# Performance work log

Measured on AMD Instinct MI355X. Metric: run time of the kernel, lower is better.

## Reference

```python
import jax, jax.numpy as jnp
import numpy as np

D_MODEL = 1024
NUM_HEADS = 16
HEAD_DIM = D_MODEL // NUM_HEADS


def setup_inputs() -> dict:
    key = jax.random.key(0)
    ks = jax.random.split(key, 9)
    B, S = 4, 2048
    scale = 1.0 / np.sqrt(D_MODEL)
    x = jax.random.normal(ks[0], (B, S, D_MODEL), dtype=jnp.float32)
    Wq = jax.random.normal(ks[1], (D_MODEL, D_MODEL), dtype=jnp.float32) * scale
    bq = jnp.zeros((D_MODEL,), dtype=jnp.float32)
    Wk = jax.random.normal(ks[2], (D_MODEL, D_MODEL), dtype=jnp.float32) * scale
    bk = jnp.zeros((D_MODEL,), dtype=jnp.float32)
    Wv = jax.random.normal(ks[3], (D_MODEL, D_MODEL), dtype=jnp.float32) * scale
    bv = jnp.zeros((D_MODEL,), dtype=jnp.float32)
    Wo = jax.random.normal(ks[4], (D_MODEL, D_MODEL), dtype=jnp.float32) * scale
    bo = jnp.zeros((D_MODEL,), dtype=jnp.float32)
    mask = jnp.ones((B, S), dtype=jnp.int32)  # 1 = attend, 0 = masked out
    return {"x": x, "mask": mask, "Wq": Wq, "bq": bq, "Wk": Wk, "bk": bk,
            "Wv": Wv, "bv": bv, "Wo": Wo, "bo": bo}


def reference(x, mask, Wq, bq, Wk, bk, Wv, bv, Wo, bo):
    B, S, D = x.shape
    H, Hd = NUM_HEADS, HEAD_DIM
    # torch Linear: y = x @ W.T + b
    q = (jnp.einsum('bsd,ed->bse', x, Wq) + bq).reshape(B, S, H, Hd).transpose(0, 2, 1, 3)
    k = (jnp.einsum('bsd,ed->bse', x, Wk) + bk).reshape(B, S, H, Hd).transpose(0, 2, 1, 3)
    v = (jnp.einsum('bsd,ed->bse', x, Wv) + bv).reshape(B, S, H, Hd).transpose(0, 2, 1, 3)
    # scaled dot-product attention with key padding mask [B,1,1,S]
    scores = jnp.einsum('bhqd,bhkd->bhqk', q, k) / jnp.sqrt(jnp.float32(Hd))
    m = mask[:, None, None, :]
    scores = jnp.where(m == 0, jnp.float32(-jnp.inf), scores)
    attn = jax.nn.softmax(scores, axis=-1)
    vals = jnp.einsum('bhqk,bhkd->bhqd', attn, v)
    vals = vals.transpose(0, 2, 1, 3).reshape(B, S, D)
    out = jnp.einsum('bsd,ed->bse', vals, Wo) + bo
    return out
```

## Files before the change

### kernel.cpp

```cpp
#include <hip/hip_runtime.h>
#include <hip/hip_bf16.h>

typedef __attribute__((ext_vector_type(8))) short short8;
typedef __attribute__((ext_vector_type(4))) short short4b;
typedef __attribute__((ext_vector_type(4))) int int4v;
typedef __attribute__((ext_vector_type(4))) float f32x4;

#define MFMA_BF16(A_, B_, C_) __builtin_amdgcn_mfma_f32_16x16x32_bf16((A_), (B_), (C_), 0, 0, 0)

#if defined(__HIP_DEVICE_COMPILE__)
#if __has_builtin(__builtin_amdgcn_exp2f)
__device__ __forceinline__ float exp2_nat(float x) { return __builtin_amdgcn_exp2f(x); }
#else
__device__ __forceinline__ float exp2_nat(float x) {
  float r;
  asm("v_exp_f32 %0, %1" : "=v"(r) : "v"(x));
  return r;
}
#endif
#else
__device__ __forceinline__ float exp2_nat(float x) { return exp2f(x); }
#endif

__device__ __forceinline__ unsigned short f2bf(float f) {
  unsigned int u = __builtin_bit_cast(unsigned int, f);
  return (unsigned short)((u + 0x7FFFu + ((u >> 16) & 1u)) >> 16);
}

__device__ __forceinline__ void gll16(const unsigned short* g, unsigned short* l) {
  __builtin_amdgcn_global_load_lds((const __attribute__((address_space(1))) void*)g,
                                   (__attribute__((address_space(3))) void*)l, 16, 0, 0);
}

#define NX (8192 * 1024)
#define NW (1024 * 1024)

__global__ void convert_k(const float* __restrict__ x,
                          const float* __restrict__ wq, const float* __restrict__ wk,
                          const float* __restrict__ wv, const float* __restrict__ wo,
                          unsigned short* __restrict__ xb,
                          unsigned short* __restrict__ wqkv,
                          unsigned short* __restrict__ wob) {
  size_t i = ((size_t)blockIdx.x * blockDim.x + threadIdx.x) * 4;
  const float* sp;
  unsigned short* dp;
  if (i < (size_t)NX) {
    sp = x + i; dp = xb + i;
  } else {
    size_t j = i - NX;
    if (j < (size_t)NW)               { sp = wq + j;            dp = wqkv + j; }
    else if (j < (size_t)(2 * NW))    { sp = wk + (j - NW);     dp = wqkv + j; }
    else if (j < (size_t)(3 * NW))    { sp = wv + (j - 2 * NW); dp = wqkv + j; }
    else                              { sp = wo + (j - 3 * NW); dp = wob + (j - 3 * NW); }
  }
  float4 v = *(const float4*)sp;
  ushort4 o;
  o.x = f2bf(v.x); o.y = f2bf(v.y); o.z = f2bf(v.z); o.w = f2bf(v.w);
  *(ushort4*)dp = o;
}

__global__ __launch_bounds__(256, 2) void gemm_qkv_k(
    const unsigned short* __restrict__ A, const unsigned short* __restrict__ Bw,
    const float* __restrict__ bq, const float* __restrict__ bk, const float* __restrict__ bv,
    unsigned short* __restrict__ qb, unsigned short* __restrict__ kb,
    unsigned short* __restrict__ vtb) {
  const int K = 1024;
  __shared__ __align__(16) unsigned short lA[128 * 32];
  __shared__ __align__(16) unsigned short lB[128 * 32];
  const int tid = threadIdx.x;
  const int lane = tid & 63;
  const int w = tid >> 6;
  const int wm = w >> 1, wn = w & 1;
  const int m0 = blockIdx.x * 128, n0 = blockIdx.y * 128;
  const int l15 = lane & 15, lg = lane >> 4;

  const f32x4 zf = {0.0f, 0.0f, 0.0f, 0.0f};
  f32x4 acc[4][4];
#pragma unroll
  for (int mi = 0; mi < 4; ++mi)
#pragma unroll
    for (int ni = 0; ni < 4; ++ni) acc[mi][ni] = zf;

  const int c0 = tid, c1 = tid + 256;
  const int r0 = c0 >> 2, k0c = (c0 & 3) * 8;
  const int r1 = c1 >> 2, k1c = (c1 & 3) * 8;
  const unsigned short* ga0 = A + (size_t)(m0 + r0) * K + k0c;
  const unsigned short* ga1 = A + (size_t)(m0 + r1) * K + k1c;
  const unsigned short* gb0 = Bw + (size_t)(n0 + r0) * K + k0c;
  const unsigned short* gb1 = Bw + (size_t)(n0 + r1) * K + k1c;

  for (int kt = 0; kt < K; kt += 32) {
    __syncthreads();
    gll16(ga0 + kt, lA + c0 * 8);
    gll16(ga1 + kt, lA + c1 * 8);
    gll16(gb0 + kt, lB + c0 * 8);
    gll16(gb1 + kt, lB + c1 * 8);
    __syncthreads();
    short8 af[4], bf[4];
#pragma unroll
    for (int mi = 0; mi < 4; ++mi)
      af[mi] = *(const short8*)&lA[(wm * 64 + mi * 16 + l15) * 32 + lg * 8];
#pragma unroll
    for (int ni = 0; ni < 4; ++ni)
      bf[ni] = *(const short8*)&lB[(wn * 64 + ni * 16 + l15) * 32 + lg * 8];
#pragma unroll
    for (int mi = 0; mi < 4; ++mi)
#pragma unroll
      for (int ni = 0; ni < 4; ++ni)
        acc[mi][ni] = MFMA_BF16(af[mi], bf[ni], acc[mi][ni]);
  }

  const int which = n0 >> 10;
  const float* bias = (which == 0) ? bq : (which == 1) ? bk : bv;
  const float qs = (which == 0) ? 0.125f * 1.44269504088896f : 1.0f;
#pragma unroll
  for (int ni = 0; ni < 4; ++ni) {
    const int n = n0 + wn * 64 + ni * 16 + l15;
    const int nn = n & 1023;
    const float bia = bias[nn];
    const int h = nn >> 6, hd = nn & 63;
#pragma unroll
    for (int mi = 0; mi < 4; ++mi) {
      const int mb = m0 + wm * 64 + mi * 16 + lg * 4;
      const int b = mb >> 11, s = mb & 2047;
      const int bh = b * 16 + h;
      if (which < 2) {
        unsigned short* dst = ((which == 0) ? qb : kb) + ((size_t)bh * 2048 + s) * 64 + hd;
#pragma unroll
        for (int r = 0; r < 4; ++r)
          dst[(size_t)r * 64] = f2bf((acc[mi][ni][r] + bia) * qs);
      } else {
        const int tle = s >> 6, w64 = s & 63;
        const int f = w64 >> 4, lgk = (w64 >> 2) & 3;
        const int kvp0 = (f >> 1) * 32 + lgk * 8 + (f & 1) * 4;
        ushort4 pk;
        pk.x = f2bf(acc[mi][ni][0] + bia);
        pk.y = f2bf(acc[mi][ni][1] + bia);
        pk.z = f2bf(acc[mi][ni][2] + bia);
        pk.w = f2bf(acc[mi][ni][3] + bia);
        *(ushort4*)(vtb + (((size_t)bh * 32 + tle) * 64 + hd) * 64 + kvp0) = pk;
      }
    }
  }
}

__global__ __launch_bounds__(256, 4) void attn_k(
    const unsigned short* __restrict__ Qb, const unsigned short* __restrict__ Kb,
    const unsigned short* __restrict__ VTb, const int* __restrict__ mask,
    unsigned short* __restrict__ vals) {
  __shared__ __align__(16) unsigned short Kl[2][64 * 64];
  __shared__ __align__(16) unsigned short Vl[2][64 * 64];
  const int tid = threadIdx.x;
  const int lane = tid & 63;
  const int w = tid >> 6;
  const int l15 = lane & 15, lg = lane >> 4;

  const int bid = blockIdx.x;
  const int wk = (bid & 7) * 128 + (bid >> 3);
  const int bh = wk >> 4, qt = wk & 15;
  const int b = bh >> 4, h = bh & 15;
  const int q0 = qt * 128 + w * 32;

  const unsigned short* Qp = Qb + (size_t)bh * (2048 * 64);
  const int* mp = mask + b * 2048;

  int mOk = 1;
  {
    const int4v* mq = (const int4v*)mp;
#pragma unroll
    for (int i = 0; i < 8; ++i) {
      int4v m = mq[lane * 8 + i];
      mOk &= (m[0] != 0) & (m[1] != 0) & (m[2] != 0) & (m[3] != 0);
    }
  }
  const bool maskAll = __all(mOk != 0);

  const int srow = tid >> 3;
  const int scol = ((tid & 7) ^ (srow & 7)) * 8;
  const unsigned short* kSrc = Kb + (size_t)bh * (2048 * 64) + srow * 64 + scol;
  const unsigned short* vSrc = VTb + (size_t)bh * (32 * 64 * 64) + srow * 64 + scol;

  short8 qf[2][2];
#pragma unroll
  for (int mi = 0; mi < 2; ++mi)
#pragma unroll
    for (int ks = 0; ks < 2; ++ks)
      qf[mi][ks] = *(const short8*)(Qp + (size_t)(q0 + mi * 16 + l15) * 64 + ks * 32 + lg * 8);

  const f32x4 zf = {0.0f, 0.0f, 0.0f, 0.0f};
  const short8 ones8 = {(short)0x3F80, (short)0x3F80, (short)0x3F80, (short)0x3F80,
                        (short)0x3F80, (short)0x3F80, (short)0x3F80, (short)0x3F80};
  f32x4 acc[2][4];
  f32x4 lsum[2];
#pragma unroll
  for (int mi = 0; mi < 2; ++mi) {
#pragma unroll
    for (int hf = 0; hf < 4; ++hf) acc[mi][hf] = zf;
    lsum[mi] = zf;
  }

  gll16(kSrc, &Kl[0][tid * 8]);
  gll16(kSrc + 2048, &Kl[0][tid * 8 + 2048]);
  gll16(vSrc, &Vl[0][tid * 8]);
  gll16(vSrc + 2048, &Vl[0][tid * 8 + 2048]);
  __syncthreads();

  for (int t = 0; t < 32; ++t) {
    const int cur = t & 1;
    if (t < 31) {
      const size_t off = (size_t)(t + 1) * 4096;
      unsigned short* kd = &Kl[cur ^ 1][tid * 8];
      unsigned short* vd = &Vl[cur ^ 1][tid * 8];
      gll16(kSrc + off, kd);
      gll16(kSrc + off + 2048, kd + 2048);
      gll16(vSrc + off, vd);
      gll16(vSrc + off + 2048, vd + 2048);
    }
    const unsigned short* Kc = Kl[cur];
    const unsigned short* Vc = Vl[cur];
    const int kv0 = t * 64;

    int4v mv[4];
    if (!maskAll) {
#pragma unroll
      for (int f = 0; f < 4; ++f) mv[f] = *(const int4v*)(mp + kv0 + f * 16 + lg * 4);
    }

    f32x4 sc[2][4];
    __builtin_amdgcn_s_setprio(1);
#pragma unroll
    for (int f = 0; f < 4; ++f) {
      short8 kf0 = *(const short8*)&Kc[(f * 16 + l15) * 64 + ((lg ^ (l15 & 7)) * 8)];
      short8 kf1 = *(const short8*)&Kc[(f * 16 + l15) * 64 + (((4 + lg) ^ (l15 & 7)) * 8)];
#pragma unroll
      for (int mi = 0; mi < 2; ++mi) {
        f32x4 tq = MFMA_BF16(kf0, qf[mi][0], zf);
        sc[mi][f] = MFMA_BF16(kf1, qf[mi][1], tq);
      }
    }
    __builtin_amdgcn_s_setprio(0);

    short8 pb[2][2];
#pragma unroll
    for (int mi = 0; mi < 2; ++mi)
#pragma unroll
      for (int f = 0; f < 4; ++f)
#pragma unroll
        for (int r = 0; r < 4; ++r) {
          float p = exp2_nat(sc[mi][f][r]);
          if (!maskAll) p = (mv[f][r] != 0) ? p : 0.0f;
          __hip_bfloat16 hb = __float2bfloat16(p);
          pb[mi][f >> 1][(f & 1) * 4 + r] = (short)__builtin_bit_cast(unsigned short, hb);
        }

    __builtin_amdgcn_s_setprio(1);
#pragma unroll
    for (int mi = 0; mi < 2; ++mi)
#pragma unroll
      for (int pr = 0; pr < 2; ++pr)
        lsum[mi] = MFMA_BF16(ones8, pb[mi][pr], lsum[mi]);
#pragma unroll
    for (int hf = 0; hf < 4; ++hf) {
#pragma unroll
      for (int pr = 0; pr < 2; ++pr) {
        short8 vv = *(const short8*)&Vc[(hf * 16 + l15) * 64 + (((pr * 4 + lg) ^ (l15 & 7)) * 8)];
#pragma unroll
        for (int mi = 0; mi < 2; ++mi)
          acc[mi][hf] = MFMA_BF16(vv, pb[mi][pr], acc[mi][hf]);
      }
    }
    __builtin_amdgcn_s_setprio(0);

    __syncthreads();
  }

#pragma unroll
  for (int mi = 0; mi < 2; ++mi) {
    float inv = 1.0f / lsum[mi][0];
    const int q = q0 + mi * 16 + l15;
    unsigned short* dst = vals + ((size_t)b * 2048 + q) * 1024 + h * 64 + lg * 4;
#pragma unroll
    for (int hf = 0; hf < 4; ++hf) {
      ushort4 o;
      o.x = f2bf(acc[mi][hf][0] * inv);
      o.y = f2bf(acc[mi][hf][1] * inv);
      o.z = f2bf(acc[mi][hf][2] * inv);
      o.w = f2bf(acc[mi][hf][3] * inv);
      *(ushort4*)(dst + hf * 16) = o;
    }
  }
}

__global__ __launch_bounds__(256, 2) void gemm_out_k(
    const unsigned short* __restrict__ A, const unsigned short* __restrict__ Bw,
    const float* __restrict__ bo, float* __restrict__ out) {
  const int K = 1024;
  __shared__ __align__(16) unsigned short lA[128 * 32];
  __shared__ __align__(16) unsigned short lB[128 * 32];
  const int tid = threadIdx.x;
  const int lane = tid & 63;
  const int w = tid >> 6;
  const int wm = w >> 1, wn = w & 1;
  const int m0 = blockIdx.x * 128, n0 = blockIdx.y * 128;
  const int l15 = lane & 15, lg = lane >> 4;

  const f32x4 zf = {0.0f, 0.0f, 0.0f, 0.0f};
  f32x4 acc[4][4];
#pragma unroll
  for (int mi = 0; mi < 4; ++mi)
#pragma unroll
    for (int ni = 0; ni < 4; ++ni) acc[mi][ni] = zf;

  const int c0 = tid, c1 = tid + 256;
  const int r0 = c0 >> 2, k0c = (c0 & 3) * 8;
  const int r1 = c1 >> 2, k1c = (c1 & 3) * 8;
  const unsigned short* ga0 = A + (size_t)(m0 + r0) * K + k0c;
  const unsigned short* ga1 = A + (size_t)(m0 + r1) * K + k1c;
  const unsigned short* gb0 = Bw + (size_t)(n0 + r0) * K + k0c;
  const unsigned short* gb1 = Bw + (size_t)(n0 + r1) * K + k1c;

  for (int kt = 0; kt < K; kt += 32) {
    __syncthreads();
    gll16(ga0 + kt, lA + c0 * 8);
    gll16(ga1 + kt, lA + c1 * 8);
    gll16(gb0 + kt, lB + c0 * 8);
    gll16(gb1 + kt, lB + c1 * 8);
    __syncthreads();
    short8 af[4], bf[4];
#pragma unroll
    for (int mi = 0; mi < 4; ++mi)
      af[mi] = *(const short8*)&lA[(wm * 64 + mi * 16 + l15) * 32 + lg * 8];
#pragma unroll
    for (int ni = 0; ni < 4; ++ni)
      bf[ni] = *(const short8*)&lB[(wn * 64 + ni * 16 + l15) * 32 + lg * 8];
#pragma unroll
    for (int mi = 0; mi < 4; ++mi)
#pragma unroll
      for (int ni = 0; ni < 4; ++ni)
        acc[mi][ni] = MFMA_BF16(af[mi], bf[ni], acc[mi][ni]);
  }

#pragma unroll
  for (int ni = 0; ni < 4; ++ni) {
    const int n = n0 + wn * 64 + ni * 16 + l15;
    const float bia = bo[n];
#pragma unroll
    for (int mi = 0; mi < 4; ++mi) {
      const int mb = m0 + wm * 64 + mi * 16 + lg * 4;
#pragma unroll
      for (int r = 0; r < 4; ++r)
        out[(size_t)(mb + r) * 1024 + n] = acc[mi][ni][r] + bia;
    }
  }
}

extern "C" void kernel_launch(void* const* d_in, const int* in_sizes, int n_in,
                              void* d_out, int out_size, void* d_ws, size_t ws_size,
                              hipStream_t stream) {
  const float* x  = (const float*)d_in[0];
  const int* mask = (const int*)d_in[1];
  const float* Wq = (const float*)d_in[2];
  const float* bq = (const float*)d_in[3];
  const float* Wk = (const float*)d_in[4];
  const float* bk = (const float*)d_in[5];
  const float* Wv = (const float*)d_in[6];
  const float* bv = (const float*)d_in[7];
  const float* Wo = (const float*)d_in[8];
  const float* bo = (const float*)d_in[9];
  float* out = (float*)d_out;

  unsigned short* xb   = (unsigned short*)d_ws;
  unsigned short* wqkv = xb + (size_t)8192 * 1024;
  unsigned short* wob  = wqkv + (size_t)3072 * 1024;
  unsigned short* qb   = wob + (size_t)1024 * 1024;
  unsigned short* kb   = qb + (size_t)64 * 2048 * 64;
  unsigned short* vtb  = kb + (size_t)64 * 2048 * 64;
  unsigned short* vals = vtb + (size_t)64 * 2048 * 64;

  convert_k<<<dim3(12288), dim3(256), 0, stream>>>(x, Wq, Wk, Wv, Wo, xb, wqkv, wob);
  gemm_qkv_k<<<dim3(64, 24), dim3(256), 0, stream>>>(xb, wqkv, bq, bk, bv, qb, kb, vtb);
  attn_k<<<dim3(1024), dim3(256), 0, stream>>>(qb, kb, vtb, mask, vals);
  gemm_out_k<<<dim3(64, 8), dim3(256), 0, stream>>>(vals, wob, bo, out);
}
```

Before: 193.8 us.

## Double GEMM K-tile to 64 with XOR-swizzled LDS layout; unroll attention loop

Both projection GEMMs now stage a 64-wide K slice per iteration instead of 32, which halves the number of barrier pairs per output tile. Global-to-LDS copies write into an XOR-swizzled column layout so the 16-lane fragment reads avoid LDS bank conflicts. The attention KV loop also gets an unroll-by-2 pragma. LDS per block doubles to 32 KB, which may limit occupancy, and the copy and compute phases are still not overlapped.

```diff
diff --git a/kernel.cpp b/kernel.cpp
--- a/kernel.cpp
+++ b/kernel.cpp
@@ -65,8 +65,8 @@
     unsigned short* __restrict__ qb, unsigned short* __restrict__ kb,
     unsigned short* __restrict__ vtb) {
   const int K = 1024;
-  __shared__ __align__(16) unsigned short lA[128 * 32];
-  __shared__ __align__(16) unsigned short lB[128 * 32];
+  __shared__ __align__(16) unsigned short lA[128 * 64];
+  __shared__ __align__(16) unsigned short lB[128 * 64];
   const int tid = threadIdx.x;
   const int lane = tid & 63;
   const int w = tid >> 6;
@@ -81,33 +81,39 @@
 #pragma unroll
     for (int ni = 0; ni < 4; ++ni) acc[mi][ni] = zf;
 
-  const int c0 = tid, c1 = tid + 256;
-  const int r0 = c0 >> 2, k0c = (c0 & 3) * 8;
-  const int r1 = c1 >> 2, k1c = (c1 & 3) * 8;
-  const unsigned short* ga0 = A + (size_t)(m0 + r0) * K + k0c;
-  const unsigned short* ga1 = A + (size_t)(m0 + r1) * K + k1c;
-  const unsigned short* gb0 = Bw + (size_t)(n0 + r0) * K + k0c;
-  const unsigned short* gb1 = Bw + (size_t)(n0 + r1) * K + k1c;
-
-  for (int kt = 0; kt < K; kt += 32) {
-    __syncthreads();
-    gll16(ga0 + kt, lA + c0 * 8);
-    gll16(ga1 + kt, lA + c1 * 8);
-    gll16(gb0 + kt, lB + c0 * 8);
-    gll16(gb1 + kt, lB + c1 * 8);
-    __syncthreads();
-    short8 af[4], bf[4];
-#pragma unroll
-    for (int mi = 0; mi < 4; ++mi)
-      af[mi] = *(const short8*)&lA[(wm * 64 + mi * 16 + l15) * 32 + lg * 8];
-#pragma unroll
-    for (int ni = 0; ni < 4; ++ni)
-      bf[ni] = *(const short8*)&lB[(wn * 64 + ni * 16 + l15) * 32 + lg * 8];
-#pragma unroll
-    for (int mi = 0; mi < 4; ++mi)
+  const int srow = tid >> 3;
+  const int scol = ((tid & 7) ^ (srow & 7)) * 8;
+  const unsigned short* gA[4];
+  const unsigned short* gB[4];
+#pragma unroll
+  for (int q = 0; q < 4; ++q) {
+    gA[q] = A + (size_t)(m0 + q * 32 + srow) * K + scol;
+    gB[q] = Bw + (size_t)(n0 + q * 32 + srow) * K + scol;
+  }
+
+  for (int kt = 0; kt < K; kt += 64) {
+    __syncthreads();
+#pragma unroll
+    for (int q = 0; q < 4; ++q) {
+      gll16(gA[q] + kt, lA + q * 2048 + tid * 8);
+      gll16(gB[q] + kt, lB + q * 2048 + tid * 8);
+    }
+    __syncthreads();
+#pragma unroll
+    for (int ks = 0; ks < 2; ++ks) {
+      short8 af[4], bf[4];
+#pragma unroll
+      for (int mi = 0; mi < 4; ++mi)
+        af[mi] = *(const short8*)&lA[(wm * 64 + mi * 16 + l15) * 64 + (((ks * 4 + lg) ^ (l15 & 7)) * 8)];
 #pragma unroll
       for (int ni = 0; ni < 4; ++ni)
-        acc[mi][ni] = MFMA_BF16(af[mi], bf[ni], acc[mi][ni]);
+        bf[ni] = *(const short8*)&lB[(wn * 64 + ni * 16 + l15) * 64 + (((ks * 4 + lg) ^ (l15 & 7)) * 8)];
+#pragma unroll
+      for (int mi = 0; mi < 4; ++mi)
+#pragma unroll
+        for (int ni = 0; ni < 4; ++ni)
+          acc[mi][ni] = MFMA_BF16(af[mi], bf[ni], acc[mi][ni]);
+    }
   }
 
   const int which = n0 >> 10;
@@ -205,6 +211,7 @@
   gll16(vSrc + 2048, &Vl[0][tid * 8 + 2048]);
   __syncthreads();
 
+#pragma unroll 2
   for (int t = 0; t < 32; ++t) {
     const int cur = t & 1;
     if (t < 31) {
@@ -295,8 +302,8 @@
     const unsigned short* __restrict__ A, const unsigned short* __restrict__ Bw,
     const float* __restrict__ bo, float* __restrict__ out) {
   const int K = 1024;
-  __shared__ __align__(16) unsigned short lA[128 * 32];
-  __shared__ __align__(16) unsigned short lB[128 * 32];
+  __shared__ __align__(16) unsigned short lA[128 * 64];
+  __shared__ __align__(16) unsigned short lB[128 * 64];
   const int tid = threadIdx.x;
   const int lane = tid & 63;
   const int w = tid >> 6;
@@ -311,33 +318,39 @@
 #pragma unroll
     for (int ni = 0; ni < 4; ++ni) acc[mi][ni] = zf;
 
-  const int c0 = tid, c1 = tid + 256;
-  const int r0 = c0 >> 2, k0c = (c0 & 3) * 8;
-  const int r1 = c1 >> 2, k1c = (c1 & 3) * 8;
-  const unsigned short* ga0 = A + (size_t)(m0 + r0) * K + k0c;
-  const unsigned short* ga1 = A + (size_t)(m0 + r1) * K + k1c;
-  const unsigned short* gb0 = Bw + (size_t)(n0 + r0) * K + k0c;
-  const unsigned short* gb1 = Bw + (size_t)(n0 + r1) * K + k1c;
-
-  for (int kt = 0; kt < K; kt += 32) {
-    __syncthreads();
-    gll16(ga0 + kt, lA + c0 * 8);
-    gll16(ga1 + kt, lA + c1 * 8);
-    gll16(gb0 + kt, lB + c0 * 8);
-    gll16(gb1 + kt, lB + c1 * 8);
-    __syncthreads();
-    short8 af[4], bf[4];
-#pragma unroll
-    for (int mi = 0; mi < 4; ++mi)
-      af[mi] = *(const short8*)&lA[(wm * 64 + mi * 16 + l15) * 32 + lg * 8];
-#pragma unroll
-    for (int ni = 0; ni < 4; ++ni)
-      bf[ni] = *(const short8*)&lB[(wn * 64 + ni * 16 + l15) * 32 + lg * 8];
-#pragma unroll
-    for (int mi = 0; mi < 4; ++mi)
+  const int srow = tid >> 3;
+  const int scol = ((tid & 7) ^ (srow & 7)) * 8;
+  const unsigned short* gA[4];
+  const unsigned short* gB[4];
+#pragma unroll
+  for (int q = 0; q < 4; ++q) {
+    gA[q] = A + (size_t)(m0 + q * 32 + srow) * K + scol;
+    gB[q] = Bw + (size_t)(n0 + q * 32 + srow) * K + scol;
+  }
+
+  for (int kt = 0; kt < K; kt += 64) {
+    __syncthreads();
+#pragma unroll
+    for (int q = 0; q < 4; ++q) {
+      gll16(gA[q] + kt, lA + q * 2048 + tid * 8);
+      gll16(gB[q] + kt, lB + q * 2048 + tid * 8);
+    }
+    __syncthreads();
+#pragma unroll
+    for (int ks = 0; ks < 2; ++ks) {
+      short8 af[4], bf[4];
+#pragma unroll
+      for (int mi = 0; mi < 4; ++mi)
+        af[mi] = *(const short8*)&lA[(wm * 64 + mi * 16 + l15) * 64 + (((ks * 4 + lg) ^ (l15 & 7)) * 8)];
 #pragma unroll
       for (int ni = 0; ni < 4; ++ni)
-        acc[mi][ni] = MFMA_BF16(af[mi], bf[ni], acc[mi][ni]);
+        bf[ni] = *(const short8*)&lB[(wn * 64 + ni * 16 + l15) * 64 + (((ks * 4 + lg) ^ (l15 & 7)) * 8)];
+#pragma unroll
+      for (int mi = 0; mi < 4; ++mi)
+#pragma unroll
+        for (int ni = 0; ni < 4; ++ni)
+          acc[mi][ni] = MFMA_BF16(af[mi], bf[ni], acc[mi][ni]);
+    }
   }
 
 #pragma unroll
```

Result: faster. 177.5 us (-8.4%).
